# Performance work log

Hardware: AMD Instinct MI355X
Metric: run time of the kernel (lower is better)

Reference implementation:

```python
import jax, jax.numpy as jnp
import numpy as np

WORD_NUMBER = 1_000_000
EMBED_SIZE = 64
BIAS_NUMBER = 5  # K = bias_number - 1 = 4 thresholds
BATCH = 8192


def setup_inputs() -> dict:
    key = jax.random.key(0)
    k1, k2, k3, k4, k5 = jax.random.split(key, 5)
    in_embed = jax.random.uniform(k1, (WORD_NUMBER, EMBED_SIZE), dtype=jnp.float32)  # torch.rand init
    in_bias = jax.random.normal(k2, (WORD_NUMBER, BIAS_NUMBER - 1), dtype=jnp.float32) * 0.1  # original init is zeros; small noise avoids degenerate thresholds
    context_id = jax.random.randint(k3, (1,), 0, WORD_NUMBER)
    target_ids = jax.random.randint(k4, (1, BATCH), 0, WORD_NUMBER)
    labels = jax.random.randint(k5, (1, BATCH), 0, BIAS_NUMBER)
    return {
        "in_embed": in_embed,
        "in_bias": in_bias,
        "context_id": context_id,
        "target_ids": target_ids,
        "labels": labels,
    }


def reference(in_embed, in_bias, context_id, target_ids, labels):
    K = in_bias.shape[1]                       # bias_number - 1
    tgt = target_ids.reshape(-1)               # (B,)
    lab = labels.reshape(-1)                   # (B,)

    ctx = in_embed[context_id]                 # (1, d) gather
    bias = in_bias[context_id]                 # (1, K) gather
    tgt_emb = in_embed[tgt]                    # (B, d) gather

    dots = tgt_emb @ ctx[0]                    # (B,) dot products
    dots_bias = dots[:, None] - bias           # (B, K)

    # predicted_labels: first j with max(dots_bias,0)==0, i.e. dots_bias<=0
    nonpos = dots_bias <= 0                    # (B, K)
    first = jnp.argmax(nonpos, axis=1)         # first True index (0 if none)
    p_labels = jnp.where(nonpos.any(axis=1), first + 1, K + 1)
    acc = jnp.mean((p_labels == lab).astype(jnp.float32))

    # generate_yt: +1 for j < label, -1 otherwise
    yt = jnp.where(jnp.arange(K)[None, :] < lab[:, None], 1.0, -1.0)  # (B, K)
    judge = dots_bias * yt
    tau = jnp.where(judge > 0, 0.0, lab[:, None].astype(jnp.float32))  # zero out correct-side entries

    bias_update = tau.mean(0)[None, :]                                  # (1, K)
    weight_update = (tau.sum(1, keepdims=True) * tgt_emb).mean(0)[None, :]  # (1, d)

    new_embed = in_embed.at[context_id].add(weight_update)   # scatter write-back
    new_bias = in_bias.at[context_id].add(-bias_update)
    return acc, new_embed, new_bias
```

## Files before the change

kernel.cpp:

```cpp
#include <hip/hip_runtime.h>
#include <hip/hip_bf16.h>

constexpr int WORDS        = 1000000;
constexpr int D            = 64;
constexpr int K            = 4;
constexpr int BATCH        = 8192;
constexpr long EMBED_ELEMS = (long)WORDS * D;
constexpr long BIAS_ELEMS  = (long)WORDS * K;
constexpr long OUT_TOTAL   = 1 + EMBED_ELEMS + BIAS_ELEMS;


__global__ void prank_compute(const float* __restrict__ in_embed,
                              const float* __restrict__ in_bias,
                              const int*   __restrict__ context_id,
                              const int*   __restrict__ target_ids,
                              const int*   __restrict__ labels,
                              float*       __restrict__ ws) {
    const int lane   = threadIdx.x & 63;
    const int wpb    = blockDim.x >> 6;
    const int wave   = blockIdx.x * wpb + (threadIdx.x >> 6);
    const int nwaves = gridDim.x * wpb;

    const int ctx = context_id[0];
    const float ce = in_embed[(size_t)ctx * D + lane];
    const float b0 = in_bias[(size_t)ctx * K + 0];
    const float b1 = in_bias[(size_t)ctx * K + 1];
    const float b2 = in_bias[(size_t)ctx * K + 2];
    const float b3 = in_bias[(size_t)ctx * K + 3];

    float cnt = 0.f, bs0 = 0.f, bs1 = 0.f, bs2 = 0.f, bs3 = 0.f, wacc = 0.f;

    for (int i = wave; i < BATCH; i += nwaves) {
        const int t   = target_ids[i];
        const int lab = labels[i];
        const float e = in_embed[(size_t)t * D + lane];
        float d = e * ce;
        #pragma unroll
        for (int off = 32; off; off >>= 1) d += __shfl_xor(d, off, 64);

        const float db0 = d - b0, db1 = d - b1, db2 = d - b2, db3 = d - b3;

        int p = K + 1;
        if (db3 <= 0.f) p = 4;
        if (db2 <= 0.f) p = 3;
        if (db1 <= 0.f) p = 2;
        if (db0 <= 0.f) p = 1;
        cnt += (p == lab) ? 1.f : 0.f;

        const float labf = (float)lab;
        const float y0 = (0 < lab) ? 1.f : -1.f;
        const float y1 = (1 < lab) ? 1.f : -1.f;
        const float y2 = (2 < lab) ? 1.f : -1.f;
        const float y3 = (3 < lab) ? 1.f : -1.f;
        const float t0 = (db0 * y0 > 0.f) ? 0.f : labf;
        const float t1 = (db1 * y1 > 0.f) ? 0.f : labf;
        const float t2 = (db2 * y2 > 0.f) ? 0.f : labf;
        const float t3 = (db3 * y3 > 0.f) ? 0.f : labf;
        bs0 += t0; bs1 += t1; bs2 += t2; bs3 += t3;
        wacc += (t0 + t1 + t2 + t3) * e;
    }

    atomicAdd(&ws[5 + lane], wacc);
    if (lane == 0) {
        atomicAdd(&ws[0], cnt);
        atomicAdd(&ws[1], bs0);
        atomicAdd(&ws[2], bs1);
        atomicAdd(&ws[3], bs2);
        atomicAdd(&ws[4], bs3);
    }
}

__global__ void prank_copy(const float* __restrict__ in_embed,
                           const float* __restrict__ in_bias,
                           float*       __restrict__ out) {
    const long n_chunks = (OUT_TOTAL - 1 - 3) / 4;
    const long c = (long)blockIdx.x * blockDim.x + threadIdx.x;
    if (c >= n_chunks) return;
    const long o = 4 + 4 * c;

    float4 v;
    if (o + 3 <= EMBED_ELEMS) {
        const float* s = in_embed + (o - 1);
        v.x = s[0]; v.y = s[1]; v.z = s[2]; v.w = s[3];
    } else if (o >= EMBED_ELEMS + 1) {
        const float* s = in_bias + (o - (EMBED_ELEMS + 1));
        v.x = s[0]; v.y = s[1]; v.z = s[2]; v.w = s[3];
    } else {
        v.x = in_embed[EMBED_ELEMS - 1];
        v.y = in_bias[0]; v.z = in_bias[1]; v.w = in_bias[2];
    }
    *reinterpret_cast<float4*>(out + o) = v;
}

__global__ void prank_fixup(const float* __restrict__ in_embed,
                            const float* __restrict__ in_bias,
                            const int*   __restrict__ context_id,
                            const float* __restrict__ ws,
                            float*       __restrict__ out) {
    const int e   = threadIdx.x;
    const int ctx = context_id[0];
    const float invB = 1.0f / (float)BATCH;

    out[1 + (size_t)ctx * D + e] = in_embed[(size_t)ctx * D + e] + ws[5 + e] * invB;

    if (e < K) {
        out[1 + EMBED_ELEMS + (size_t)ctx * K + e] =
            in_bias[(size_t)ctx * K + e] - ws[1 + e] * invB;
    }
    if (e == 0) out[0] = ws[0] * invB;

    if (e >= 1 && e <= 3) {
        float v = in_embed[e - 1];
        if (ctx == 0) v += ws[5 + (e - 1)] * invB;
        out[e] = v;
    }
    if (e == 4) {
        float v = in_bias[BIAS_ELEMS - 1];
        if (ctx == WORDS - 1) v -= ws[4] * invB;
        out[OUT_TOTAL - 1] = v;
    }
}

extern "C" void kernel_launch(void* const* d_in, const int* in_sizes, int n_in,
                              void* d_out, int out_size, void* d_ws, size_t ws_size,
                              hipStream_t stream) {
    const float* in_embed   = (const float*)d_in[0];
    const float* in_bias    = (const float*)d_in[1];
    const int*   context_id = (const int*)d_in[2];
    const int*   target_ids = (const int*)d_in[3];
    const int*   labels     = (const int*)d_in[4];
    float* out = (float*)d_out;
    float* ws  = (float*)d_ws;

    hipMemsetAsync(ws, 0, (5 + D) * sizeof(float), stream);

    prank_compute<<<64, 256, 0, stream>>>(in_embed, in_bias, context_id,
                                          target_ids, labels, ws);

    const long n_chunks = (OUT_TOTAL - 1 - 3) / 4;
    const int  blocks   = (int)((n_chunks + 255) / 256);
    prank_copy<<<blocks, 256, 0, stream>>>(in_embed, in_bias, out);

    prank_fixup<<<1, 64, 0, stream>>>(in_embed, in_bias, context_id, ws, out);
}
```

Measured before the change: 492.2 us.

## Fuse compute and copy kernels, replace atomics with per-block partials

Merges the batch reduction and the bulk table copy into one launch: the first 64 blocks run the ordinal-regression reduction, and the remaining blocks perform the float4 copy. The copy now uses a single memcpy-based unaligned 4-float load instead of four scalar loads. Global atomics and the workspace memset are replaced by per-block partial sums written to workspace, which the fixup kernel reduces serially. This removes one launch plus the memset, and lets the small compute run alongside the bandwidth-bound copy, in exchange for a slightly longer fixup.

```diff
diff --git a/kernel.cpp b/kernel.cpp
--- a/kernel.cpp
+++ b/kernel.cpp
@@ -9,87 +9,97 @@
 constexpr long BIAS_ELEMS  = (long)WORDS * K;
 constexpr long OUT_TOTAL   = 1 + EMBED_ELEMS + BIAS_ELEMS;
 
+constexpr int  CBLK     = 64;
+constexpr int  SLOTS    = 69;
+constexpr long N_CHUNKS = (OUT_TOTAL - 1 - 3) / 4;
 
-__global__ void prank_compute(const float* __restrict__ in_embed,
-                              const float* __restrict__ in_bias,
-                              const int*   __restrict__ context_id,
-                              const int*   __restrict__ target_ids,
-                              const int*   __restrict__ labels,
-                              float*       __restrict__ ws) {
-    const int lane   = threadIdx.x & 63;
-    const int wpb    = blockDim.x >> 6;
-    const int wave   = blockIdx.x * wpb + (threadIdx.x >> 6);
-    const int nwaves = gridDim.x * wpb;
 
-    const int ctx = context_id[0];
-    const float ce = in_embed[(size_t)ctx * D + lane];
-    const float b0 = in_bias[(size_t)ctx * K + 0];
-    const float b1 = in_bias[(size_t)ctx * K + 1];
-    const float b2 = in_bias[(size_t)ctx * K + 2];
-    const float b3 = in_bias[(size_t)ctx * K + 3];
-
-    float cnt = 0.f, bs0 = 0.f, bs1 = 0.f, bs2 = 0.f, bs3 = 0.f, wacc = 0.f;
-
-    for (int i = wave; i < BATCH; i += nwaves) {
-        const int t   = target_ids[i];
-        const int lab = labels[i];
-        const float e = in_embed[(size_t)t * D + lane];
-        float d = e * ce;
-        #pragma unroll
-        for (int off = 32; off; off >>= 1) d += __shfl_xor(d, off, 64);
-
-        const float db0 = d - b0, db1 = d - b1, db2 = d - b2, db3 = d - b3;
-
-        int p = K + 1;
-        if (db3 <= 0.f) p = 4;
-        if (db2 <= 0.f) p = 3;
-        if (db1 <= 0.f) p = 2;
-        if (db0 <= 0.f) p = 1;
-        cnt += (p == lab) ? 1.f : 0.f;
-
-        const float labf = (float)lab;
-        const float y0 = (0 < lab) ? 1.f : -1.f;
-        const float y1 = (1 < lab) ? 1.f : -1.f;
-        const float y2 = (2 < lab) ? 1.f : -1.f;
-        const float y3 = (3 < lab) ? 1.f : -1.f;
-        const float t0 = (db0 * y0 > 0.f) ? 0.f : labf;
-        const float t1 = (db1 * y1 > 0.f) ? 0.f : labf;
-        const float t2 = (db2 * y2 > 0.f) ? 0.f : labf;
-        const float t3 = (db3 * y3 > 0.f) ? 0.f : labf;
-        bs0 += t0; bs1 += t1; bs2 += t2; bs3 += t3;
-        wacc += (t0 + t1 + t2 + t3) * e;
-    }
-
-    atomicAdd(&ws[5 + lane], wacc);
-    if (lane == 0) {
-        atomicAdd(&ws[0], cnt);
-        atomicAdd(&ws[1], bs0);
-        atomicAdd(&ws[2], bs1);
-        atomicAdd(&ws[3], bs2);
-        atomicAdd(&ws[4], bs3);
-    }
+__device__ inline float4 load4_unaligned(const float* p) {
+    float4 v;
+    __builtin_memcpy(&v, p, sizeof(float4));
+    return v;
 }
 
-__global__ void prank_copy(const float* __restrict__ in_embed,
-                           const float* __restrict__ in_bias,
-                           float*       __restrict__ out) {
-    const long n_chunks = (OUT_TOTAL - 1 - 3) / 4;
-    const long c = (long)blockIdx.x * blockDim.x + threadIdx.x;
-    if (c >= n_chunks) return;
-    const long o = 4 + 4 * c;
+__global__ void prank_fused(const float* __restrict__ in_embed,
+                            const float* __restrict__ in_bias,
+                            const int*   __restrict__ context_id,
+                            const int*   __restrict__ target_ids,
+                            const int*   __restrict__ labels,
+                            float*       __restrict__ ws,
+                            float*       __restrict__ out) {
+    if (blockIdx.x < CBLK) {
+        __shared__ float part[4][SLOTS];
+        const int lane = threadIdx.x & 63;
+        const int w    = threadIdx.x >> 6;
+        const int wave = blockIdx.x * 4 + w;
 
-    float4 v;
-    if (o + 3 <= EMBED_ELEMS) {
-        const float* s = in_embed + (o - 1);
-        v.x = s[0]; v.y = s[1]; v.z = s[2]; v.w = s[3];
-    } else if (o >= EMBED_ELEMS + 1) {
-        const float* s = in_bias + (o - (EMBED_ELEMS + 1));
-        v.x = s[0]; v.y = s[1]; v.z = s[2]; v.w = s[3];
+        const int ctx = context_id[0];
+        const float ce = in_embed[(size_t)ctx * D + lane];
+        const float b0 = in_bias[(size_t)ctx * K + 0];
+        const float b1 = in_bias[(size_t)ctx * K + 1];
+        const float b2 = in_bias[(size_t)ctx * K + 2];
+        const float b3 = in_bias[(size_t)ctx * K + 3];
+
+        float cnt = 0.f, bs0 = 0.f, bs1 = 0.f, bs2 = 0.f, bs3 = 0.f, wacc = 0.f;
+
+        for (int i = wave; i < BATCH; i += CBLK * 4) {
+            const int t   = target_ids[i];
+            const int lab = labels[i];
+            const float e = in_embed[(size_t)t * D + lane];
+            float d = e * ce;
+            #pragma unroll
+            for (int off = 32; off; off >>= 1) d += __shfl_xor(d, off, 64);
+
+            const float db0 = d - b0, db1 = d - b1, db2 = d - b2, db3 = d - b3;
+
+            int p = K + 1;
+            if (db3 <= 0.f) p = 4;
+            if (db2 <= 0.f) p = 3;
+            if (db1 <= 0.f) p = 2;
+            if (db0 <= 0.f) p = 1;
+            cnt += (p == lab) ? 1.f : 0.f;
+
+            const float labf = (float)lab;
+            const float y0 = (0 < lab) ? 1.f : -1.f;
+            const float y1 = (1 < lab) ? 1.f : -1.f;
+            const float y2 = (2 < lab) ? 1.f : -1.f;
+            const float y3 = (3 < lab) ? 1.f : -1.f;
+            const float t0 = (db0 * y0 > 0.f) ? 0.f : labf;
+            const float t1 = (db1 * y1 > 0.f) ? 0.f : labf;
+            const float t2 = (db2 * y2 > 0.f) ? 0.f : labf;
+            const float t3 = (db3 * y3 > 0.f) ? 0.f : labf;
+            bs0 += t0; bs1 += t1; bs2 += t2; bs3 += t3;
+            wacc += (t0 + t1 + t2 + t3) * e;
+        }
+
+        part[w][5 + lane] = wacc;
+        if (lane == 0) {
+            part[w][0] = cnt;
+            part[w][1] = bs0; part[w][2] = bs1;
+            part[w][3] = bs2; part[w][4] = bs3;
+        }
+        __syncthreads();
+        if (threadIdx.x < SLOTS) {
+            const int t = threadIdx.x;
+            ws[(size_t)blockIdx.x * SLOTS + t] =
+                part[0][t] + part[1][t] + part[2][t] + part[3][t];
+        }
     } else {
-        v.x = in_embed[EMBED_ELEMS - 1];
-        v.y = in_bias[0]; v.z = in_bias[1]; v.w = in_bias[2];
+        const long c = (long)(blockIdx.x - CBLK) * blockDim.x + threadIdx.x;
+        if (c >= N_CHUNKS) return;
+        const long o = 4 + 4 * c;
+
+        float4 v;
+        if (o + 3 <= EMBED_ELEMS) {
+            v = load4_unaligned(in_embed + (o - 1));
+        } else if (o >= EMBED_ELEMS + 1) {
+            v = load4_unaligned(in_bias + (o - (EMBED_ELEMS + 1)));
+        } else {
+            v.x = in_embed[EMBED_ELEMS - 1];
+            v.y = in_bias[0]; v.z = in_bias[1]; v.w = in_bias[2];
+        }
+        *reinterpret_cast<float4*>(out + o) = v;
     }
-    *reinterpret_cast<float4*>(out + o) = v;
 }
 
 __global__ void prank_fixup(const float* __restrict__ in_embed,
@@ -97,26 +107,38 @@
                             const int*   __restrict__ context_id,
                             const float* __restrict__ ws,
                             float*       __restrict__ out) {
-    const int e   = threadIdx.x;
+    __shared__ float s[SLOTS];
+    const int e = threadIdx.x;
+
+    float wsum = 0.f;
+    for (int b = 0; b < CBLK; ++b) wsum += ws[(size_t)b * SLOTS + 5 + e];
+    s[5 + e] = wsum;
+    if (e < 5) {
+        float a = 0.f;
+        for (int b = 0; b < CBLK; ++b) a += ws[(size_t)b * SLOTS + e];
+        s[e] = a;
+    }
+    __syncthreads();
+
     const int ctx = context_id[0];
     const float invB = 1.0f / (float)BATCH;
 
-    out[1 + (size_t)ctx * D + e] = in_embed[(size_t)ctx * D + e] + ws[5 + e] * invB;
+    out[1 + (size_t)ctx * D + e] = in_embed[(size_t)ctx * D + e] + s[5 + e] * invB;
 
-    if (e < K) {
-        out[1 + EMBED_ELEMS + (size_t)ctx * K + e] =
-            in_bias[(size_t)ctx * K + e] - ws[1 + e] * invB;
+    if (e >= 1 && e <= 4) {
+        out[1 + EMBED_ELEMS + (size_t)ctx * K + (e - 1)] =
+            in_bias[(size_t)ctx * K + (e - 1)] - s[e] * invB;
     }
-    if (e == 0) out[0] = ws[0] * invB;
+    if (e == 0) out[0] = s[0] * invB;
 
     if (e >= 1 && e <= 3) {
         float v = in_embed[e - 1];
-        if (ctx == 0) v += ws[5 + (e - 1)] * invB;
+        if (ctx == 0) v += s[5 + (e - 1)] * invB;
         out[e] = v;
     }
-    if (e == 4) {
+    if (e == 5) {
         float v = in_bias[BIAS_ELEMS - 1];
-        if (ctx == WORDS - 1) v -= ws[4] * invB;
+        if (ctx == WORDS - 1) v -= s[4] * invB;
         out[OUT_TOTAL - 1] = v;
     }
 }
@@ -132,14 +154,9 @@
     float* out = (float*)d_out;
     float* ws  = (float*)d_ws;
 
-    hipMemsetAsync(ws, 0, (5 + D) * sizeof(float), stream);
-
-    prank_compute<<<64, 256, 0, stream>>>(in_embed, in_bias, context_id,
-                                          target_ids, labels, ws);
-
-    const long n_chunks = (OUT_TOTAL - 1 - 3) / 4;
-    const int  blocks   = (int)((n_chunks + 255) / 256);
-    prank_copy<<<blocks, 256, 0, stream>>>(in_embed, in_bias, out);
+    const int copy_blocks = (int)((N_CHUNKS + 255) / 256);
+    prank_fused<<<CBLK + copy_blocks, 256, 0, stream>>>(
+        in_embed, in_bias, context_id, target_ids, labels, ws, out);
 
     prank_fixup<<<1, 64, 0, stream>>>(in_embed, in_bias, context_id, ws, out);
 }
```

New measurement: 440.0 us. 10.6% less time.
